# Kernel optimization log

Hardware: AMD Instinct MI355X
Metric: run time of the kernel (lower is better)

## Reference

```python
import jax, jax.numpy as jnp
import numpy as np


def batch_pairwise_dist(x, y):
    # x: [B, N, D], y: [B, M, D] -> P: [B, N, M] squared distances
    xx = jnp.sum(x * x, axis=-1)            # [B, N]
    yy = jnp.sum(y * y, axis=-1)            # [B, M]
    zz = jnp.einsum('bnd,bmd->bnm', x, y)   # [B, N, M]
    return xx[:, :, None] + yy[:, None, :] - 2.0 * zz


def setup_inputs() -> dict:
    key = jax.random.key(0)
    k1, k2 = jax.random.split(key)
    B, N, M, D = 8, 8192, 8192, 3
    preds = jax.random.normal(k1, (B, M, D), dtype=jnp.float32)
    gts = jax.random.normal(k2, (B, N, D), dtype=jnp.float32)
    return {"preds": preds, "gts": gts}


def reference(preds, gts):
    P = batch_pairwise_dist(gts, preds)     # [B, N, M]
    loss_1 = jnp.sum(jnp.min(P, axis=1))    # min over gts points
    loss_2 = jnp.sum(jnp.min(P, axis=2))    # min over preds points
    return loss_1 + loss_2
```

## Files before the change

kernel.cpp:

```cpp
#include <hip/hip_runtime.h>
#include <hip/hip_bf16.h>

#define BATCH 8
#define NPTS  8192
#define NPT_TOT (BATCH * NPTS)

typedef __attribute__((ext_vector_type(8)))  short short8;
typedef __attribute__((ext_vector_type(16))) float float16;
typedef unsigned int uint32;

__device__ __forceinline__ uint32 map_f(float f) {
    int i = __float_as_int(f);
    return (uint32)(i ^ ((i >> 31) | 0x80000000));
}
__device__ __forceinline__ float unmap_f(uint32 u) {
    int i = (u & 0x80000000u) ? (int)(u ^ 0x80000000u) : (int)~u;
    return __int_as_float(i);
}

__device__ __forceinline__ unsigned short bf16_of(float f) {
    __hip_bfloat16 h = __float2bfloat16(f);
    return *reinterpret_cast<unsigned short*>(&h);
}
__device__ __forceinline__ float f_of_bf16(unsigned short u) {
    __hip_bfloat16 h = *reinterpret_cast<__hip_bfloat16*>(&u);
    return __bfloat162float(h);
}
__device__ __forceinline__ uint32 pk(unsigned short lo, unsigned short hi) {
    return (uint32)lo | ((uint32)hi << 16);
}
__device__ __forceinline__ float max3f(float a, float b, float c) {
    float d;
    asm("v_max3_f32 %0, %1, %2, %3" : "=v"(d) : "v"(a), "v"(b), "v"(c));
    return d;
}

__global__ __launch_bounds__(256)
void prepass(const float* __restrict__ gts, const float* __restrict__ preds,
             float* __restrict__ norms, uint32* __restrict__ smax,
             unsigned short* __restrict__ AG, unsigned short* __restrict__ BG,
             unsigned short* __restrict__ AP, unsigned short* __restrict__ BP)
{
    int i = blockIdx.x * blockDim.x + threadIdx.x;
    if (i >= 2 * NPT_TOT) return;
    const bool isGt = i < NPT_TOT;
    const int j = isGt ? i : i - NPT_TOT;
    const float* src = (isGt ? gts : preds) + 3 * (size_t)j;
    const float x = src[0], y = src[1], z = src[2];
    const float h = 0.5f * (x * x + y * y + z * z);
    norms[i] = h;
    smax[i]  = 0u;

    const unsigned short xh = bf16_of(x), yh = bf16_of(y), zh = bf16_of(z);
    const unsigned short xl = bf16_of(x - f_of_bf16(xh));
    const unsigned short yl = bf16_of(y - f_of_bf16(yh));
    const unsigned short zl = bf16_of(z - f_of_bf16(zh));
    const unsigned short nhh = bf16_of(-h);
    const unsigned short nhl = bf16_of(-h - f_of_bf16(nhh));
    const unsigned short one = 0x3F80;

    unsigned short* A = (isGt ? AG : AP) + (size_t)j * 16;
    uint4 av0 = { pk(xh, yh), pk(zh, xl), pk(yl, zl), pk(xh, yh) };
    uint4 av1 = { pk(zh, xl), pk(yl, zl), pk(one, one), 0u };
    *reinterpret_cast<uint4*>(A)     = av0;
    *reinterpret_cast<uint4*>(A + 8) = av1;

    const int b = j >> 13;
    const int q = j & 8191;
    const int t = q >> 5, p = q & 31;
    unsigned short* Bf = (isGt ? BG : BP) + ((size_t)b * 16384 + t * 64 + p) * 8;
    uint4 bv0 = { pk(xh, yh), pk(zh, xh), pk(yh, zh), pk(xl, yl) };
    uint4 bv1 = { pk(zl, xl), pk(yl, zl), pk(nhh, nhl), 0u };
    *reinterpret_cast<uint4*>(Bf)            = bv0;
    *reinterpret_cast<uint4*>(Bf + 32 * 8)   = bv1;
}

#define MFMA_V(D, Asrc, Bsrc, Csrc)                                          \
    asm volatile("v_mfma_f32_32x32x16_bf16 %0, %1, %2, %3"                   \
                 : "=&v"(D) : "v"(Asrc), "v"(Bsrc), "v"(Csrc))

#define RED8(d, mx)                                   \
    {  mx = max3f(d[0],  d[1],  mx);                  \
       mx = max3f(d[2],  d[3],  mx);                  \
       mx = max3f(d[4],  d[5],  mx);                  \
       mx = max3f(d[6],  d[7],  mx);                  \
       mx = max3f(d[8],  d[9],  mx);                  \
       mx = max3f(d[10], d[11], mx);                  \
       mx = max3f(d[12], d[13], mx);                  \
       mx = max3f(d[14], d[15], mx); }

#define CT 16

__global__ __launch_bounds__(256, 4)
void chamfer_mfma(const unsigned short* __restrict__ AG,
                  const unsigned short* __restrict__ BP,
                  const unsigned short* __restrict__ AP,
                  const unsigned short* __restrict__ BG,
                  uint32* __restrict__ smax_all)
{
    __shared__ short8 sb[CT * 64];

    const int tid   = threadIdx.x;
    const int lane  = tid & 63;
    const int wid   = tid >> 6;
    const int dir   = blockIdx.z >> 3;
    const int batch = blockIdx.z & 7;
    const int row0  = blockIdx.y * 512 + wid * 128;

    const unsigned short* Arows = dir ? AP : AG;
    const unsigned short* Bcols = dir ? BG : BP;
    uint32* smax = smax_all + dir * NPT_TOT;

    const int lr = lane & 31, lg = lane >> 5;

    const short8* gB = reinterpret_cast<const short8*>(Bcols)
                     + (size_t)batch * 16384 + (size_t)blockIdx.x * (CT * 64);
#pragma unroll
    for (int s = 0; s < 4; ++s) sb[s * 256 + tid] = gB[s * 256 + tid];

    const short8* gA = reinterpret_cast<const short8*>(Arows);
    const size_t abase = ((size_t)batch * NPTS + row0 + lr) * 2 + lg;
    const short8 a0 = gA[abase];
    const short8 a1 = gA[abase + 64];
    const short8 a2 = gA[abase + 128];
    const short8 a3 = gA[abase + 192];

    float16 z16 = {0.f, 0.f, 0.f, 0.f, 0.f, 0.f, 0.f, 0.f,
                   0.f, 0.f, 0.f, 0.f, 0.f, 0.f, 0.f, 0.f};
    float mx0 = -INFINITY, mx1 = -INFINITY, mx2 = -INFINITY, mx3 = -INFINITY;

    __syncthreads();

    for (int tt = 0; tt < CT; ++tt) {
        const short8 bv = sb[tt * 64 + lane];

        float16 d0, d1;
        MFMA_V(d0, bv, a0, z16);
        MFMA_V(d1, bv, a1, z16);
        asm volatile("s_nop 7\n\ts_nop 7" : "+v"(d0), "+v"(d1));
        RED8(d0, mx0);
        RED8(d1, mx1);

        MFMA_V(d0, bv, a2, z16);
        MFMA_V(d1, bv, a3, z16);
        asm volatile("s_nop 7\n\ts_nop 7" : "+v"(d0), "+v"(d1));
        RED8(d0, mx2);
        RED8(d1, mx3);
    }

    mx0 = fmaxf(mx0, __shfl_xor(mx0, 32, 64));
    mx1 = fmaxf(mx1, __shfl_xor(mx1, 32, 64));
    mx2 = fmaxf(mx2, __shfl_xor(mx2, 32, 64));
    mx3 = fmaxf(mx3, __shfl_xor(mx3, 32, 64));
    if (lane < 32) {
        uint32* s = smax + batch * NPTS + row0 + lane;
        atomicMax(s,      map_f(mx0));
        atomicMax(s + 32, map_f(mx1));
        atomicMax(s + 64, map_f(mx2));
        atomicMax(s + 96, map_f(mx3));
    }
}

__global__ __launch_bounds__(256)
void final_stage1(const float* __restrict__ norms, const uint32* __restrict__ smax,
                  float* __restrict__ partials)
{
    const int base = blockIdx.x * 1024;
    float s = 0.f;
    for (int k = threadIdx.x; k < 1024; k += 256) {
        const int i = base + k;
        s += norms[i] - unmap_f(smax[i]);
    }
#pragma unroll
    for (int off = 32; off; off >>= 1) s += __shfl_down(s, off, 64);
    __shared__ float ws4[4];
    if ((threadIdx.x & 63) == 0) ws4[threadIdx.x >> 6] = s;
    __syncthreads();
    if (threadIdx.x == 0) partials[blockIdx.x] = (ws4[0] + ws4[1]) + (ws4[2] + ws4[3]);
}

__global__ void final_stage2(const float* __restrict__ partials, float* __restrict__ out)
{
    float s = partials[threadIdx.x] + partials[threadIdx.x + 64];
#pragma unroll
    for (int off = 32; off; off >>= 1) s += __shfl_down(s, off, 64);
    if (threadIdx.x == 0) *out = 2.0f * s;
}

extern "C" void kernel_launch(void* const* d_in, const int* in_sizes, int n_in,
                              void* d_out, int out_size, void* d_ws, size_t ws_size,
                              hipStream_t stream) {
    const float* preds = (const float*)d_in[0];
    const float* gts   = (const float*)d_in[1];

    char* w = (char*)d_ws;
    float*  norms = (float*)w;
    uint32* smax  = (uint32*)(w + 8 * (size_t)NPT_TOT);
    const size_t PITCH = 32 * (size_t)NPT_TOT;
    unsigned short* AG = (unsigned short*)(w + 16 * (size_t)NPT_TOT);
    unsigned short* BG = (unsigned short*)((char*)AG + PITCH);
    unsigned short* AP = (unsigned short*)((char*)AG + 2 * PITCH);
    unsigned short* BP = (unsigned short*)((char*)AG + 3 * PITCH);
    float* partials = (float*)((char*)AG + 4 * PITCH);

    prepass<<<(2 * NPT_TOT) / 256, 256, 0, stream>>>(gts, preds, norms, smax,
                                                     AG, BG, AP, BP);

    dim3 grid(16, 16, 16);
    chamfer_mfma<<<grid, 256, 0, stream>>>(AG, BP, AP, BG, smax);

    final_stage1<<<128, 256, 0, stream>>>(norms, smax, partials);
    final_stage2<<<1, 64, 0, stream>>>(partials, (float*)d_out);
}
```

Measured before the change: 50.72 us.

## Software-pipeline MFMA with max reduction and halve rows per wave

Each wave now handles 64 rows instead of 128, and the grid doubles in y to keep total work the same. The inner loop is software-pipelined with two accumulator pairs, so the MFMAs for the next column tile are issued before the max3 reduction of the previous tile's results. This is meant to hide MFMA latency behind the VALU reductions rather than stalling on s_nop waits. In exchange, twice as many blocks reload the shared B tile and issue atomics, which adds LDS fill and global traffic.

```diff
diff --git a/kernel.cpp b/kernel.cpp
--- a/kernel.cpp
+++ b/kernel.cpp
@@ -105,7 +105,7 @@
     const int wid   = tid >> 6;
     const int dir   = blockIdx.z >> 3;
     const int batch = blockIdx.z & 7;
-    const int row0  = blockIdx.y * 512 + wid * 128;
+    const int row0  = blockIdx.y * 256 + wid * 64;
 
     const unsigned short* Arows = dir ? AP : AG;
     const unsigned short* Bcols = dir ? BG : BP;
@@ -122,42 +122,53 @@
     const size_t abase = ((size_t)batch * NPTS + row0 + lr) * 2 + lg;
     const short8 a0 = gA[abase];
     const short8 a1 = gA[abase + 64];
-    const short8 a2 = gA[abase + 128];
-    const short8 a3 = gA[abase + 192];
 
     float16 z16 = {0.f, 0.f, 0.f, 0.f, 0.f, 0.f, 0.f, 0.f,
                    0.f, 0.f, 0.f, 0.f, 0.f, 0.f, 0.f, 0.f};
-    float mx0 = -INFINITY, mx1 = -INFINITY, mx2 = -INFINITY, mx3 = -INFINITY;
+    float mx0 = -INFINITY, mx1 = -INFINITY;
 
     __syncthreads();
 
-    for (int tt = 0; tt < CT; ++tt) {
-        const short8 bv = sb[tt * 64 + lane];
-
-        float16 d0, d1;
-        MFMA_V(d0, bv, a0, z16);
-        MFMA_V(d1, bv, a1, z16);
-        asm volatile("s_nop 7\n\ts_nop 7" : "+v"(d0), "+v"(d1));
-        RED8(d0, mx0);
-        RED8(d1, mx1);
-
-        MFMA_V(d0, bv, a2, z16);
-        MFMA_V(d1, bv, a3, z16);
-        asm volatile("s_nop 7\n\ts_nop 7" : "+v"(d0), "+v"(d1));
-        RED8(d0, mx2);
-        RED8(d1, mx3);
+    float16 dA0, dA1, dB0, dB1;
+    {
+        const short8 bv = sb[lane];
+        MFMA_V(dA0, bv, a0, z16);
+        MFMA_V(dA1, bv, a1, z16);
+    }
+
+    for (int tt = 0; tt < CT - 2; tt += 2) {
+        const short8 bvo = sb[(tt + 1) * 64 + lane];
+        MFMA_V(dB0, bvo, a0, z16);
+        MFMA_V(dB1, bvo, a1, z16);
+        asm volatile("s_nop 7\n\ts_nop 7" : "+v"(dA0), "+v"(dA1));
+        RED8(dA0, mx0);
+        RED8(dA1, mx1);
+
+        const short8 bve = sb[(tt + 2) * 64 + lane];
+        MFMA_V(dA0, bve, a0, z16);
+        MFMA_V(dA1, bve, a1, z16);
+        asm volatile("s_nop 7\n\ts_nop 7" : "+v"(dB0), "+v"(dB1));
+        RED8(dB0, mx0);
+        RED8(dB1, mx1);
+    }
+    {
+        const short8 bvo = sb[(CT - 1) * 64 + lane];
+        MFMA_V(dB0, bvo, a0, z16);
+        MFMA_V(dB1, bvo, a1, z16);
+        asm volatile("s_nop 7\n\ts_nop 7" : "+v"(dA0), "+v"(dA1));
+        RED8(dA0, mx0);
+        RED8(dA1, mx1);
+        asm volatile("s_nop 7\n\ts_nop 7" : "+v"(dB0), "+v"(dB1));
+        RED8(dB0, mx0);
+        RED8(dB1, mx1);
     }
 
     mx0 = fmaxf(mx0, __shfl_xor(mx0, 32, 64));
     mx1 = fmaxf(mx1, __shfl_xor(mx1, 32, 64));
-    mx2 = fmaxf(mx2, __shfl_xor(mx2, 32, 64));
-    mx3 = fmaxf(mx3, __shfl_xor(mx3, 32, 64));
     if (lane < 32) {
         uint32* s = smax + batch * NPTS + row0 + lane;
         atomicMax(s,      map_f(mx0));
         atomicMax(s + 32, map_f(mx1));
-        atomicMax(s + 64, map_f(mx2));
-        atomicMax(s + 96, map_f(mx3));
     }
 }
 
@@ -206,7 +217,7 @@
     prepass<<<(2 * NPT_TOT) / 256, 256, 0, stream>>>(gts, preds, norms, smax,
                                                      AG, BG, AP, BP);
 
-    dim3 grid(16, 16, 16);
+    dim3 grid(16, 32, 16);
     chamfer_mfma<<<grid, 256, 0, stream>>>(AG, BP, AP, BG, smax);
 
     final_stage1<<<128, 256, 0, stream>>>(norms, smax, partials);
```

New measurement: 53.28 us. 5.0% more time.
